# Performance work log

Hardware: AMD Instinct MI355X
Metric: run time of the kernel (lower is better)

The kernel has to match this reference:

```python
import jax, jax.numpy as jnp
import numpy as np

EPS = 1e-5
NUM_HEADS = 16
TEMP = 0.01

def _ln(x, g, b):
    m = jnp.mean(x, axis=-1, keepdims=True)
    v = jnp.var(x, axis=-1, keepdims=True)
    return (x - m) * jax.lax.rsqrt(v + EPS) * g + b

def setup_inputs() -> dict:
    key = jax.random.key(0)
    ks = jax.random.split(key, 16)
    b, l, c, ni = 4, 1024, 1024, 2
    d = c // NUM_HEADS
    s = lambda fan: 1.0 / np.sqrt(fan)
    return {
        "x_list": jax.random.normal(ks[0], (b, l, c, ni), jnp.float32),
        "w_": jax.random.normal(ks[1], (4 + ni, 1), jnp.float32),
        "qkv_w": jax.random.normal(ks[2], (3 * c, c), jnp.float32) * s(c),
        "qkv_b": jax.random.normal(ks[3], (3 * c,), jnp.float32) * 0.02,
        "proj_w": jax.random.normal(ks[4], (c, c), jnp.float32) * s(c),
        "proj_b": jax.random.normal(ks[5], (c,), jnp.float32) * 0.02,
        "nq_g": jnp.ones((d,), jnp.float32),
        "nq_b": jnp.zeros((d,), jnp.float32),
        "nk_g": jnp.ones((d,), jnp.float32),
        "nk_b": jnp.zeros((d,), jnp.float32),
        "conv_w": jax.random.normal(ks[6], (c, c), jnp.float32) * s(c),
        "conv_b": jax.random.normal(ks[7], (c,), jnp.float32) * 0.02,
        "ca1_w": jax.random.normal(ks[8], (c // 16, c), jnp.float32) * s(c),
        "ca1_b": jax.random.normal(ks[9], (c // 16,), jnp.float32) * 0.02,
        "ca2_w": jax.random.normal(ks[10], (c, c // 16), jnp.float32) * s(c // 16),
        "ca2_b": jax.random.normal(ks[11], (c,), jnp.float32) * 0.02,
        "mlp1_w": jax.random.normal(ks[12], (4 * c, c), jnp.float32) * s(c),
        "mlp1_b": jax.random.normal(ks[13], (4 * c,), jnp.float32) * 0.02,
        "mlp2_w": jax.random.normal(ks[14], (c, 4 * c), jnp.float32) * s(4 * c),
        "mlp2_b": jax.random.normal(ks[15], (c,), jnp.float32) * 0.02,
    }

def reference(x_list, w_, qkv_w, qkv_b, proj_w, proj_b, nq_g, nq_b, nk_g, nk_b,
              conv_w, conv_b, ca1_w, ca1_b, ca2_w, ca2_b, mlp1_w, mlp1_b, mlp2_w, mlp2_b):
    x = x_list[..., -1]  # [b, l, c]
    # op 0: Conv1x1Act = GELU(Linear)
    op0 = jax.nn.gelu(x @ conv_w.T + conv_b, approximate=False)
    # op 1: ChannelAttention = sigmoid(fc2(relu(fc1(x)))) * x
    op1 = jax.nn.sigmoid(jax.nn.relu(x @ ca1_w.T + ca1_b) @ ca2_w.T + ca2_b) * x
    # op 2: Identity
    op2 = x
    # op 3: MLP = fc2(GELU(fc1(x)))
    op3 = jax.nn.gelu(x @ mlp1_w.T + mlp1_b, approximate=False) @ mlp2_w.T + mlp2_b
    new = jnp.stack([op0, op1, op2, op3], axis=-1)  # [b, l, c, 4]
    xc = jnp.concatenate([x_list, new], axis=-1)    # [b, l, c, ni+4]
    w = jax.nn.softmax(w_ / TEMP, axis=0)           # [ni+4, 1]
    x = jnp.einsum('blcn,ni->blci', xc, w)[..., 0]  # [b, l, c]
    x_res = x
    # attention with per-head LayerNorm on q, k
    b_, n, c = x.shape
    d = c // NUM_HEADS
    qkv = x @ qkv_w.T + qkv_b
    q, k, v = jnp.split(qkv, 3, axis=-1)
    to_heads = lambda t: t.reshape(b_, n, NUM_HEADS, d).transpose(0, 2, 1, 3)  # [b, h, n, d]
    q, k, v = to_heads(q), to_heads(k), to_heads(v)
    q = _ln(q, nq_g, nq_b)
    k = _ln(k, nk_g, nk_b)
    score = jnp.einsum('bhnd,bhmd->bhnm', q, k) / np.sqrt(d).astype(np.float32)
    attn = jax.nn.softmax(score, axis=-1)           # [b, h, n, n]
    attn_map = attn.mean(axis=1)[:, 0, 1:]          # [b, n-1]
    out = jnp.einsum('bhnm,bhmd->bhnd', attn, v)
    out = out.transpose(0, 2, 1, 3).reshape(b_, n, c)
    out = out @ proj_w.T + proj_b + x_res
    return out, attn_map
```

## Files before the change

kernel.cpp:

```cpp
#include <hip/hip_runtime.h>
#include <hip/hip_bf16.h>

typedef __attribute__((ext_vector_type(8))) short short8;
typedef __attribute__((ext_vector_type(4))) float f32x4;

#define MROWS 4096
#define CDIM  1024
#define HEADS 16
#define DHEAD 64
#define NSEQ  1024

__device__ inline float softw(const float* __restrict__ w, int idx) {
    float m = w[0];
#pragma unroll
    for (int i = 1; i < 6; i++) m = fmaxf(m, w[i]);
    float s = 0.f, v = 0.f;
#pragma unroll
    for (int i = 0; i < 6; i++) {
        float e = __expf((w[i] - m) * 100.0f);
        s += e;
        if (i == idx) v = e;
    }
    return v / s;
}

__device__ inline float gelu_f(float x) {
    return 0.5f * x * (1.0f + erff(x * 0.70710678118654752f));
}

__global__ __launch_bounds__(256) void mix_base(
    const float* __restrict__ x_list, __hip_bfloat16* __restrict__ xb,
    float* __restrict__ am_acc)
{
    int i2 = blockIdx.x * 256 + threadIdx.x;
    float4 v = ((const float4*)x_list)[i2];
    __hip_bfloat162 o;
    o.x = __float2bfloat16(v.y);
    o.y = __float2bfloat16(v.w);
    ((__hip_bfloat162*)xb)[i2] = o;
    if (i2 < 4096) am_acc[i2] = 0.f;
}

__global__ __launch_bounds__(256) void f2b_all(
    const float* __restrict__ conv_w, const float* __restrict__ mlp1_w,
    const float* __restrict__ qkv_w, const float* __restrict__ proj_w,
    const float* __restrict__ mlp2_w, const float* __restrict__ ca1_w,
    __hip_bfloat16* __restrict__ wcat, __hip_bfloat16* __restrict__ qkvwb,
    __hip_bfloat16* __restrict__ projwb, __hip_bfloat16* __restrict__ mlp2wb)
{
    size_t e = ((size_t)blockIdx.x * 256 + threadIdx.x) * 4;
    const float* src; __hip_bfloat16* dst; size_t o;
    if (e < 1048576)       { src = conv_w; dst = wcat;           o = e; }
    else if (e < 5242880)  { src = mlp1_w; dst = wcat + 1048576; o = e - 1048576; }
    else if (e < 5308416)  { src = ca1_w;  dst = wcat + 5242880; o = e - 5242880; }
    else if (e < 5373952) {
        __hip_bfloat162 z; z.x = __float2bfloat16(0.f); z.y = z.x;
        __hip_bfloat16* d = wcat + 5308416 + (e - 5308416);
        *(__hip_bfloat162*)(d)     = z;
        *(__hip_bfloat162*)(d + 2) = z;
        return;
    }
    else if (e < 8519680)  { src = qkv_w;  dst = qkvwb;          o = e - 5373952; }
    else if (e < 9568256)  { src = proj_w; dst = projwb;         o = e - 8519680; }
    else                   { src = mlp2_w; dst = mlp2wb;         o = e - 9568256; }
    float4 v = *(const float4*)(src + o);
    __hip_bfloat162 a, b;
    a.x = __float2bfloat16(v.x); a.y = __float2bfloat16(v.y);
    b.x = __float2bfloat16(v.z); b.y = __float2bfloat16(v.w);
    *(__hip_bfloat162*)(dst + o)     = a;
    *(__hip_bfloat162*)(dst + o + 2) = b;
}

#define BKT 32
#define LDA 40

template<int EPI, int FM, int FN, int SWZ>
__global__ __launch_bounds__(256) void gemm_bf16(
    const __hip_bfloat16* __restrict__ A, const __hip_bfloat16* __restrict__ W,
    const float* __restrict__ bias,
    float* __restrict__ f0, const float* __restrict__ f1,
    __hip_bfloat16* __restrict__ b0, __hip_bfloat16* __restrict__ b1,
    __hip_bfloat16* __restrict__ b2,
    const float* __restrict__ g0, const float* __restrict__ be0,
    const float* __restrict__ g1, const float* __restrict__ be1,
    const float* __restrict__ wvec, int M, int N, int K)
{
    constexpr int BMt = FM * 32;
    constexpr int BNt = FN * 32;
    constexpr int NA = BMt / 64;
    constexpr int NB = BNt / 64;
    __shared__ __hip_bfloat16 As[2][BMt * LDA];
    __shared__ __hip_bfloat16 Bs[2][BNt * LDA];
    int t = threadIdx.x;
    int bx = blockIdx.x, by = blockIdx.y;
    if constexpr (SWZ) {
        int nx = gridDim.x;
        int lin = by * nx + bx;
        int cpx = (nx * gridDim.y) >> 3;
        int swz = (lin & 7) * cpx + (lin >> 3);
        bx = swz % nx;
        by = swz / nx;
    }
    int n0 = bx * BNt, m0 = by * BMt;
    int wave = t >> 6, lane = t & 63;
    int wr = wave >> 1, wc = wave & 1;
    int quad = lane >> 4, l16 = lane & 15;
    int r0 = t >> 2, c0 = (t & 3) * 8;

    short8 sa0[NA], sb0[NB], sa1[NA], sb1[NB];
    auto ldg = [&](int k0, short8* da, short8* db) {
#pragma unroll
        for (int i = 0; i < NA; i++)
            da[i] = *(const short8*)(A + (size_t)(m0 + r0 + 64 * i) * K + k0 + c0);
#pragma unroll
        for (int i = 0; i < NB; i++)
            db[i] = *(const short8*)(W + (size_t)(n0 + r0 + 64 * i) * K + k0 + c0);
    };
    ldg(0, sa0, sb0);
    ldg(BKT, sa1, sb1);

    f32x4 zero = {0.f, 0.f, 0.f, 0.f};
    f32x4 acc[FM][FN];
#pragma unroll
    for (int i = 0; i < FM; i++)
#pragma unroll
        for (int j = 0; j < FN; j++) acc[i][j] = zero;

    for (int k0 = 0; k0 < K; k0 += 2 * BKT) {
#pragma unroll
        for (int i = 0; i < NA; i++)
            *(short8*)&As[0][(r0 + 64 * i) * LDA + c0] = sa0[i];
#pragma unroll
        for (int i = 0; i < NB; i++)
            *(short8*)&Bs[0][(r0 + 64 * i) * LDA + c0] = sb0[i];
        __syncthreads();
        if (k0 + 2 * BKT < K) ldg(k0 + 2 * BKT, sa0, sb0);
        {
            short8 af[FM], bf[FN];
#pragma unroll
            for (int i = 0; i < FM; i++)
                af[i] = *(const short8*)&As[0][(wr * FM * 16 + i * 16 + l16) * LDA + quad * 8];
#pragma unroll
            for (int j = 0; j < FN; j++)
                bf[j] = *(const short8*)&Bs[0][(wc * FN * 16 + j * 16 + l16) * LDA + quad * 8];
#pragma unroll
            for (int i = 0; i < FM; i++)
#pragma unroll
                for (int j = 0; j < FN; j++)
                    acc[i][j] = __builtin_amdgcn_mfma_f32_16x16x32_bf16(
                        af[i], bf[j], acc[i][j], 0, 0, 0);
        }
#pragma unroll
        for (int i = 0; i < NA; i++)
            *(short8*)&As[1][(r0 + 64 * i) * LDA + c0] = sa1[i];
#pragma unroll
        for (int i = 0; i < NB; i++)
            *(short8*)&Bs[1][(r0 + 64 * i) * LDA + c0] = sb1[i];
        __syncthreads();
        if (k0 + 3 * BKT < K) ldg(k0 + 3 * BKT, sa1, sb1);
        {
            short8 af[FM], bf[FN];
#pragma unroll
            for (int i = 0; i < FM; i++)
                af[i] = *(const short8*)&As[1][(wr * FM * 16 + i * 16 + l16) * LDA + quad * 8];
#pragma unroll
            for (int j = 0; j < FN; j++)
                bf[j] = *(const short8*)&Bs[1][(wc * FN * 16 + j * 16 + l16) * LDA + quad * 8];
#pragma unroll
            for (int i = 0; i < FM; i++)
#pragma unroll
                for (int j = 0; j < FN; j++)
                    acc[i][j] = __builtin_amdgcn_mfma_f32_16x16x32_bf16(
                        af[i], bf[j], acc[i][j], 0, 0, 0);
        }
    }

    if constexpr (EPI == 1) {
        float wmx = softw(wvec, 2);
        float w0c = softw(wvec, 0);
        float w14c = softw(wvec, 1) + softw(wvec, 4);
        int colbase = n0 + wc * FN * 16;
        int region = (colbase < 1024) ? 0 : (colbase < 5120) ? 1
                   : (colbase < 5184) ? 2 : 3;
        if (region == 3) return;
#pragma unroll
        for (int i = 0; i < FM; i++) {
#pragma unroll
            for (int j = 0; j < FN; j++) {
                int col = colbase + j * 16 + l16;
                float bv = (region == 0) ? bias[col]
                         : (region == 1) ? be0[col - 1024]
                                         : g0[col - 5120];
#pragma unroll
                for (int r = 0; r < 4; r++) {
                    int row = m0 + wr * FM * 16 + i * 16 + quad * 4 + r;
                    float v = acc[i][j][r] + bv;
                    if (region == 0) {
                        size_t idx = (size_t)row * 1024 + col;
                        float2 xl = ((const float2*)f1)[idx];
                        b0[idx] = __float2bfloat16(
                            w0c * xl.x + w14c * xl.y + wmx * gelu_f(v));
                    } else if (region == 1) {
                        b1[(size_t)row * 4096 + (col - 1024)] =
                            __float2bfloat16(gelu_f(v));
                    } else {
                        f0[(size_t)row * 64 + (col - 5120)] = fmaxf(v, 0.f);
                    }
                }
            }
        }
        return;
    }

    if constexpr (EPI == 5) {
        int colbase = n0 + wc * FN * 16;
        int portion = colbase >> 10;
        int hh = (colbase >> 6) & 15;
        float bv[FN];
#pragma unroll
        for (int j = 0; j < FN; j++) bv[j] = bias[colbase + j * 16 + l16];
        if (portion == 2) {
#pragma unroll
            for (int i = 0; i < FM; i++)
#pragma unroll
                for (int j = 0; j < FN; j++)
#pragma unroll
                    for (int r = 0; r < 4; r++) {
                        int row = m0 + wr * FM * 16 + i * 16 + quad * 4 + r;
                        int bb = row >> 10, nn = row & 1023;
                        int dd = j * 16 + l16;
                        b0[((size_t)(bb * 16 + hh) * DHEAD + dd) * NSEQ + nn] =
                            __float2bfloat16(acc[i][j][r] + bv[j]);
                    }
        } else {
            const float* g  = (portion == 0) ? g0 : g1;
            const float* be = (portion == 0) ? be0 : be1;
            __hip_bfloat16* dst = (portion == 0) ? b1 : b2;
            float qs = (portion == 0) ? 0.125f : 1.0f;
            float gv[FN], bev[FN];
#pragma unroll
            for (int j = 0; j < FN; j++) {
                gv[j] = g[j * 16 + l16] * qs;
                bev[j] = be[j * 16 + l16] * qs;
            }
#pragma unroll
            for (int i = 0; i < FM; i++)
#pragma unroll
                for (int r = 0; r < 4; r++) {
                    float s1 = 0.f, s2 = 0.f;
#pragma unroll
                    for (int j = 0; j < FN; j++) {
                        float v = acc[i][j][r] + bv[j];
                        s1 += v; s2 += v * v;
                    }
#pragma unroll
                    for (int mk = 1; mk < 16; mk <<= 1) {
                        s1 += __shfl_xor(s1, mk, 64);
                        s2 += __shfl_xor(s2, mk, 64);
                    }
                    float mean = s1 * (1.f / 64.f);
                    float var = s2 * (1.f / 64.f) - mean * mean;
                    float rs = rsqrtf(var + 1e-5f);
                    int row = m0 + wr * FM * 16 + i * 16 + quad * 4 + r;
                    int bb = row >> 10, nn = row & 1023;
                    size_t base = ((size_t)(bb * 16 + hh) * NSEQ + nn) * DHEAD;
#pragma unroll
                    for (int j = 0; j < FN; j++)
                        dst[base + j * 16 + l16] = __float2bfloat16(
                            (acc[i][j][r] + bv[j] - mean) * rs * gv[j] + bev[j]);
                }
        }
        return;
    }

    float wmx = 0.f;
    if (EPI == 3) wmx = softw(wvec, 5);

#pragma unroll
    for (int i = 0; i < FM; i++) {
#pragma unroll
        for (int j = 0; j < FN; j++) {
            int col = n0 + wc * FN * 16 + j * 16 + l16;
            float bv = bias[col];
#pragma unroll
            for (int r = 0; r < 4; r++) {
                int row = m0 + wr * FM * 16 + i * 16 + quad * 4 + r;
                float v = acc[i][j][r] + bv;
                size_t idx = (size_t)row * N + col;
                if (EPI == 3) {
                    float tv = __bfloat162float(b0[idx]) + wmx * v;
                    b0[idx] = __float2bfloat16(tv);
                } else if (EPI == 4) {
                    f0[idx] = v + __bfloat162float(b1[idx]);
                }
            }
        }
    }
}

__global__ __launch_bounds__(256) void ca2_kernel(
    const float* __restrict__ h1, const float* __restrict__ w,
    const float* __restrict__ bias, const __hip_bfloat16* __restrict__ xb,
    __hip_bfloat16* __restrict__ xmixb, const float* __restrict__ wvec)
{
    __shared__ float Wt[256 * 65];
    __shared__ float hs[16 * 64];
    int t = threadIdx.x;
    int m0 = blockIdx.x * 16, n0 = blockIdx.y * 256;
#pragma unroll
    for (int i = 0; i < 64; i++) {
        int e = t + i * 256; int r = e >> 6, c = e & 63;
        Wt[r * 65 + c] = w[(size_t)(n0 + r) * 64 + c];
    }
#pragma unroll
    for (int i = 0; i < 4; i++) {
        int e = t + i * 256; int r = e >> 6, c = e & 63;
        hs[r * 64 + c] = h1[(size_t)(m0 + r) * 64 + c];
    }
    __syncthreads();
    int n = n0 + t;
    float bv = bias[n];
    float acc[16];
#pragma unroll
    for (int mi = 0; mi < 16; mi++) acc[mi] = bv;
    for (int k = 0; k < 64; k++) {
        float wv = Wt[t * 65 + k];
#pragma unroll
        for (int mi = 0; mi < 16; mi++) acc[mi] += hs[mi * 64 + k] * wv;
    }
    float w3 = softw(wvec, 3);
#pragma unroll
    for (int mi = 0; mi < 16; mi++) {
        size_t idx = (size_t)(m0 + mi) * 1024 + n;
        float sg = 1.f / (1.f + __expf(-acc[mi]));
        float cur = __bfloat162float(xmixb[idx]);
        xmixb[idx] = __float2bfloat16(cur + w3 * sg * __bfloat162float(xb[idx]));
    }
}

#define PSTR 72
__global__ __launch_bounds__(256) void flash_mfma(
    const __hip_bfloat16* __restrict__ qb, const __hip_bfloat16* __restrict__ kb,
    const __hip_bfloat16* __restrict__ vt, __hip_bfloat16* __restrict__ ao)
{
    __shared__ __hip_bfloat16 Plds[4][32 * PSTR];
    int l = blockIdx.y * 64 + blockIdx.x;
    int swz = (l & 7) * 64 + (l >> 3);
    int bh = swz >> 3;
    int i0 = (swz & 7) * 128;
    int b = bh >> 4, h = bh & 15;
    int t = threadIdx.x, wave = t >> 6, lane = t & 63;
    int l16 = lane & 15, quad = lane >> 4;
    const __hip_bfloat16* qbase = qb + (size_t)bh * NSEQ * DHEAD;
    const __hip_bfloat16* kbase = kb + (size_t)bh * NSEQ * DHEAD;
    const __hip_bfloat16* vbase = vt + (size_t)bh * DHEAD * NSEQ;
    __hip_bfloat16* pw = Plds[wave];
    int qrow0 = i0 + wave * 32;

    short8 aq[2][2];
#pragma unroll
    for (int ri = 0; ri < 2; ri++)
#pragma unroll
        for (int ks = 0; ks < 2; ks++)
            aq[ri][ks] = *(const short8*)(qbase +
                (size_t)(qrow0 + ri * 16 + l16) * DHEAD + ks * 32 + quad * 8);

    f32x4 zero = {0.f, 0.f, 0.f, 0.f};
    f32x4 o[2][4];
    float lrow[2][4];
#pragma unroll
    for (int ri = 0; ri < 2; ri++) {
#pragma unroll
        for (int nt = 0; nt < 4; nt++) o[ri][nt] = zero;
#pragma unroll
        for (int rr = 0; rr < 4; rr++) lrow[ri][rr] = 0.f;
    }

    for (int j0 = 0; j0 < NSEQ; j0 += 64) {
        short8 bk[4][2];
#pragma unroll
        for (int jt = 0; jt < 4; jt++)
#pragma unroll
            for (int ks = 0; ks < 2; ks++)
                bk[jt][ks] = *(const short8*)(kbase +
                    (size_t)(j0 + jt * 16 + l16) * DHEAD + ks * 32 + quad * 8);
        short8 bv[4][2];
#pragma unroll
        for (int nt = 0; nt < 4; nt++)
#pragma unroll
            for (int ks = 0; ks < 2; ks++)
                bv[nt][ks] = *(const short8*)(vbase +
                    (size_t)(nt * 16 + l16) * NSEQ + j0 + ks * 32 + quad * 8);

#pragma unroll
        for (int ri = 0; ri < 2; ri++) {
            f32x4 s[4];
#pragma unroll
            for (int jt = 0; jt < 4; jt++) s[jt] = zero;
#pragma unroll
            for (int jt = 0; jt < 4; jt++)
#pragma unroll
                for (int ks = 0; ks < 2; ks++)
                    s[jt] = __builtin_amdgcn_mfma_f32_16x16x32_bf16(
                        aq[ri][ks], bk[jt][ks], s[jt], 0, 0, 0);
#pragma unroll
            for (int rr = 0; rr < 4; rr++) {
                float ss = 0.f;
#pragma unroll
                for (int jt = 0; jt < 4; jt++) {
                    float p = __expf(s[jt][rr]);
                    pw[(ri * 16 + quad * 4 + rr) * PSTR + jt * 16 + l16] =
                        __float2bfloat16(p);
                    ss += p;
                }
#pragma unroll
                for (int mk = 1; mk < 16; mk <<= 1) ss += __shfl_xor(ss, mk, 64);
                lrow[ri][rr] += ss;
            }
        }
#pragma unroll
        for (int ri = 0; ri < 2; ri++) {
            short8 ap[2];
#pragma unroll
            for (int ks = 0; ks < 2; ks++)
                ap[ks] = *(const short8*)&pw[(ri * 16 + l16) * PSTR + ks * 32 + quad * 8];
#pragma unroll
            for (int nt = 0; nt < 4; nt++)
#pragma unroll
                for (int ks = 0; ks < 2; ks++)
                    o[ri][nt] = __builtin_amdgcn_mfma_f32_16x16x32_bf16(
                        ap[ks], bv[nt][ks], o[ri][nt], 0, 0, 0);
        }
    }

#pragma unroll
    for (int ri = 0; ri < 2; ri++)
#pragma unroll
        for (int rr = 0; rr < 4; rr++) {
            float inv = 1.f / lrow[ri][rr];
            int row = qrow0 + ri * 16 + quad * 4 + rr;
#pragma unroll
            for (int nt = 0; nt < 4; nt++)
                ao[((size_t)b * NSEQ + row) * CDIM + h * 64 + nt * 16 + l16] =
                    __float2bfloat16(o[ri][nt][rr] * inv);
        }
}

__global__ __launch_bounds__(256) void attn_map_acc(
    const __hip_bfloat16* __restrict__ qf, const __hip_bfloat16* __restrict__ kf,
    float* __restrict__ am)
{
    __shared__ float q0[64];
    __shared__ float red[256];
    int bh = blockIdx.x, t = threadIdx.x;
    const __hip_bfloat16* qr = qf + (size_t)bh * NSEQ * DHEAD;
    const __hip_bfloat16* kb = kf + (size_t)bh * NSEQ * DHEAD;
    if (t < 64) q0[t] = __bfloat162float(qr[t]);
    __syncthreads();
    float s[4];
    float mx = -1e30f;
#pragma unroll
    for (int ji = 0; ji < 4; ji++) {
        int j = ji * 256 + t;
        float a = 0.f;
        for (int k = 0; k < 64; k++) a += q0[k] * __bfloat162float(kb[(size_t)j * 64 + k]);
        s[ji] = a;
        mx = fmaxf(mx, a);
    }
    red[t] = mx; __syncthreads();
    for (int st = 128; st > 0; st >>= 1) {
        if (t < st) red[t] = fmaxf(red[t], red[t + st]);
        __syncthreads();
    }
    float M = red[0]; __syncthreads();
    float sum = 0.f;
#pragma unroll
    for (int ji = 0; ji < 4; ji++) { s[ji] = __expf(s[ji] - M); sum += s[ji]; }
    red[t] = sum; __syncthreads();
    for (int st = 128; st > 0; st >>= 1) {
        if (t < st) red[t] += red[t + st];
        __syncthreads();
    }
    float inv = 1.f / red[0];
    int b = bh >> 4;
#pragma unroll
    for (int ji = 0; ji < 4; ji++) {
        int j = ji * 256 + t;
        if (j > 0) atomicAdd(&am[b * 1024 + j], s[ji] * inv * (1.f / 16.f));
    }
}

__global__ __launch_bounds__(256) void attn_map_out(
    const float* __restrict__ am, float* __restrict__ out1)
{
    int i = blockIdx.x * 256 + threadIdx.x;
    if (i < 4 * 1023) {
        int b = i / 1023;
        int j = i - b * 1023 + 1;
        out1[i] = am[b * 1024 + j];
    }
}

extern "C" void kernel_launch(void* const* d_in, const int* in_sizes, int n_in,
                              void* d_out, int out_size, void* d_ws, size_t ws_size,
                              hipStream_t stream)
{
    const float* x_list = (const float*)d_in[0];
    const float* wvec   = (const float*)d_in[1];
    const float* qkv_w  = (const float*)d_in[2];
    const float* qkv_b  = (const float*)d_in[3];
    const float* proj_w = (const float*)d_in[4];
    const float* proj_b = (const float*)d_in[5];
    const float* nq_g   = (const float*)d_in[6];
    const float* nq_b   = (const float*)d_in[7];
    const float* nk_g   = (const float*)d_in[8];
    const float* nk_b   = (const float*)d_in[9];
    const float* conv_w = (const float*)d_in[10];
    const float* conv_b = (const float*)d_in[11];
    const float* ca1_w  = (const float*)d_in[12];
    const float* ca1_b  = (const float*)d_in[13];
    const float* ca2_w  = (const float*)d_in[14];
    const float* ca2_b  = (const float*)d_in[15];
    const float* mlp1_w = (const float*)d_in[16];
    const float* mlp1_b = (const float*)d_in[17];
    const float* mlp2_w = (const float*)d_in[18];
    const float* mlp2_b = (const float*)d_in[19];

    float* out0 = (float*)d_out;
    float* out1 = out0 + (size_t)4 * 1024 * 1024;

    char* ws = (char*)d_ws;
    size_t off = 0;
    auto alloc = [&](size_t bytes) -> char* {
        char* p = ws + off;
        off += (bytes + 255) & ~(size_t)255;
        return p;
    };
    __hip_bfloat16* xb     = (__hip_bfloat16*)alloc((size_t)MROWS * CDIM * 2);
    __hip_bfloat16* xmixb  = (__hip_bfloat16*)alloc((size_t)MROWS * CDIM * 2);
    float*          h1     = (float*)alloc((size_t)MROWS * 64 * 4);
    __hip_bfloat16* hb     = (__hip_bfloat16*)alloc((size_t)MROWS * 4096 * 2);
    __hip_bfloat16* qbb    = (__hip_bfloat16*)alloc((size_t)MROWS * CDIM * 2);
    __hip_bfloat16* kbb    = (__hip_bfloat16*)alloc((size_t)MROWS * CDIM * 2);
    __hip_bfloat16* vtb    = (__hip_bfloat16*)alloc((size_t)MROWS * CDIM * 2);
    __hip_bfloat16* aob    = (__hip_bfloat16*)alloc((size_t)MROWS * CDIM * 2);
    float*          amacc  = (float*)alloc(4096 * 4);
    __hip_bfloat16* wcat   = (__hip_bfloat16*)alloc((size_t)5248 * 1024 * 2);
    __hip_bfloat16* qkvwb  = (__hip_bfloat16*)alloc((size_t)3145728 * 2);
    __hip_bfloat16* projwb = (__hip_bfloat16*)alloc((size_t)1048576 * 2);
    __hip_bfloat16* mlp2wb = (__hip_bfloat16*)alloc((size_t)4194304 * 2);

    f2b_all<<<13440, 256, 0, stream>>>(conv_w, mlp1_w, qkv_w, proj_w, mlp2_w,
                                       ca1_w, wcat, qkvwb, projwb, mlp2wb);

    mix_base<<<8192, 256, 0, stream>>>(x_list, xb, amacc);

    gemm_bf16<1, 4, 4, 0><<<dim3(41, 32), 256, 0, stream>>>(
        xb, wcat, conv_b, h1, x_list, xmixb, hb, nullptr,
        ca1_b, mlp1_b, nullptr, nullptr, wvec, MROWS, 5248, 1024);

    ca2_kernel<<<dim3(256, 4), 256, 0, stream>>>(h1, ca2_w, ca2_b, xb, xmixb, wvec);

    gemm_bf16<3, 2, 4, 1><<<dim3(8, 64), 256, 0, stream>>>(
        hb, mlp2wb, mlp2_b, nullptr, nullptr, xmixb, nullptr, nullptr,
        nullptr, nullptr, nullptr, nullptr, wvec, MROWS, 1024, 4096);

    gemm_bf16<5, 4, 4, 1><<<dim3(24, 32), 256, 0, stream>>>(
        xmixb, qkvwb, qkv_b, nullptr, nullptr, vtb, qbb, kbb,
        nq_g, nq_b, nk_g, nk_b, wvec, MROWS, 3072, 1024);

    flash_mfma<<<dim3(64, 8), 256, 0, stream>>>(qbb, kbb, vtb, aob);

    attn_map_acc<<<64, 256, 0, stream>>>(qbb, kbb, amacc);
    attn_map_out<<<16, 256, 0, stream>>>(amacc, out1);

    gemm_bf16<4, 2, 4, 1><<<dim3(8, 64), 256, 0, stream>>>(
        aob, projwb, proj_b, out0, nullptr, nullptr, xmixb, nullptr,
        nullptr, nullptr, nullptr, nullptr, wvec, MROWS, 1024, 1024);
}
```

Before: 482.9 us.

## Fold log2e into Q scale, compute softmax row sums via MFMA

Folds log2(e) into the query scaling so the attention kernels use exp2f instead of __expf. The per-row softmax denominator no longer uses a shuffle reduction; it is computed by an extra MFMA against a ones column appended to V and then broadcast from the lane holding it. The first GEMM launch also switches to a 1D grid with a custom mapping that schedules the 40 full column tiles first and the narrow last column tile at the end. This trades cross-lane reduction work for one more MFMA per tile, at the cost of a few extra accumulator registers.

```diff
diff --git a/kernel.cpp b/kernel.cpp
--- a/kernel.cpp
+++ b/kernel.cpp
@@ -93,13 +93,18 @@
     __shared__ __hip_bfloat16 Bs[2][BNt * LDA];
     int t = threadIdx.x;
     int bx = blockIdx.x, by = blockIdx.y;
-    if constexpr (SWZ) {
+    if constexpr (SWZ == 1) {
         int nx = gridDim.x;
         int lin = by * nx + bx;
         int cpx = (nx * gridDim.y) >> 3;
         int swz = (lin & 7) * cpx + (lin >> 3);
         bx = swz % nx;
         by = swz / nx;
+    }
+    if constexpr (SWZ == 2) {
+        int l = blockIdx.x;
+        if (l < 1280) { bx = l % 40; by = l / 40; }
+        else          { bx = 40;     by = l - 1280; }
     }
     int n0 = bx * BNt, m0 = by * BMt;
     int wave = t >> 6, lane = t & 63;
@@ -236,7 +241,7 @@
             const float* g  = (portion == 0) ? g0 : g1;
             const float* be = (portion == 0) ? be0 : be1;
             __hip_bfloat16* dst = (portion == 0) ? b1 : b2;
-            float qs = (portion == 0) ? 0.125f : 1.0f;
+            float qs = (portion == 0) ? 0.125f * 1.4426950408889634f : 1.0f;
             float gv[FN], bev[FN];
 #pragma unroll
             for (int j = 0; j < FN; j++) {
@@ -365,16 +370,19 @@
             aq[ri][ks] = *(const short8*)(qbase +
                 (size_t)(qrow0 + ri * 16 + l16) * DHEAD + ks * 32 + quad * 8);
 
+    short8 bones;
+    {
+        short fill = (l16 == 0) ? (short)0x3F80 : (short)0;
+#pragma unroll
+        for (int z = 0; z < 8; z++) bones[z] = fill;
+    }
+
     f32x4 zero = {0.f, 0.f, 0.f, 0.f};
-    f32x4 o[2][4];
-    float lrow[2][4];
-#pragma unroll
-    for (int ri = 0; ri < 2; ri++) {
-#pragma unroll
-        for (int nt = 0; nt < 4; nt++) o[ri][nt] = zero;
-#pragma unroll
-        for (int rr = 0; rr < 4; rr++) lrow[ri][rr] = 0.f;
-    }
+    f32x4 o[2][5];
+#pragma unroll
+    for (int ri = 0; ri < 2; ri++)
+#pragma unroll
+        for (int nt = 0; nt < 5; nt++) o[ri][nt] = zero;
 
     for (int j0 = 0; j0 < NSEQ; j0 += 64) {
         short8 bk[4][2];
@@ -404,19 +412,11 @@
                     s[jt] = __builtin_amdgcn_mfma_f32_16x16x32_bf16(
                         aq[ri][ks], bk[jt][ks], s[jt], 0, 0, 0);
 #pragma unroll
-            for (int rr = 0; rr < 4; rr++) {
-                float ss = 0.f;
-#pragma unroll
-                for (int jt = 0; jt < 4; jt++) {
-                    float p = __expf(s[jt][rr]);
+            for (int rr = 0; rr < 4; rr++)
+#pragma unroll
+                for (int jt = 0; jt < 4; jt++)
                     pw[(ri * 16 + quad * 4 + rr) * PSTR + jt * 16 + l16] =
-                        __float2bfloat16(p);
-                    ss += p;
-                }
-#pragma unroll
-                for (int mk = 1; mk < 16; mk <<= 1) ss += __shfl_xor(ss, mk, 64);
-                lrow[ri][rr] += ss;
-            }
+                        __float2bfloat16(exp2f(s[jt][rr]));
         }
 #pragma unroll
         for (int ri = 0; ri < 2; ri++) {
@@ -425,11 +425,11 @@
             for (int ks = 0; ks < 2; ks++)
                 ap[ks] = *(const short8*)&pw[(ri * 16 + l16) * PSTR + ks * 32 + quad * 8];
 #pragma unroll
-            for (int nt = 0; nt < 4; nt++)
+            for (int nt = 0; nt < 5; nt++)
 #pragma unroll
                 for (int ks = 0; ks < 2; ks++)
                     o[ri][nt] = __builtin_amdgcn_mfma_f32_16x16x32_bf16(
-                        ap[ks], bv[nt][ks], o[ri][nt], 0, 0, 0);
+                        ap[ks], (nt == 4) ? bones : bv[nt][ks], o[ri][nt], 0, 0, 0);
         }
     }
 
@@ -437,7 +437,8 @@
     for (int ri = 0; ri < 2; ri++)
 #pragma unroll
         for (int rr = 0; rr < 4; rr++) {
-            float inv = 1.f / lrow[ri][rr];
+            float lsum = __shfl(o[ri][4][rr], quad << 4, 64);
+            float inv = 1.f / lsum;
             int row = qrow0 + ri * 16 + quad * 4 + rr;
 #pragma unroll
             for (int nt = 0; nt < 4; nt++)
@@ -475,7 +476,7 @@
     float M = red[0]; __syncthreads();
     float sum = 0.f;
 #pragma unroll
-    for (int ji = 0; ji < 4; ji++) { s[ji] = __expf(s[ji] - M); sum += s[ji]; }
+    for (int ji = 0; ji < 4; ji++) { s[ji] = exp2f(s[ji] - M); sum += s[ji]; }
     red[t] = sum; __syncthreads();
     for (int st = 128; st > 0; st >>= 1) {
         if (t < st) red[t] += red[t + st];
@@ -555,7 +556,7 @@
 
     mix_base<<<8192, 256, 0, stream>>>(x_list, xb, amacc);
 
-    gemm_bf16<1, 4, 4, 0><<<dim3(41, 32), 256, 0, stream>>>(
+    gemm_bf16<1, 4, 4, 2><<<1312, 256, 0, stream>>>(
         xb, wcat, conv_b, h1, x_list, xmixb, hb, nullptr,
         ca1_b, mlp1_b, nullptr, nullptr, wvec, MROWS, 5248, 1024);
 
```

Result: slower. 566.4 us (+17.3%).
